# Kernel optimization log

Hardware: AMD Instinct MI355X
Metric: run time of the kernel (lower is better)

## Reference

```python
import jax, jax.numpy as jnp
import numpy as np

N = 100000        # vertices
E = 20000         # hyperedges
NNZ = 1000000     # incidence pairs
IN_CH = 128
HEADS = 8
OUT_CH = 16
D = HEADS * OUT_CH  # 128
NUM_TYPES = 16
K_CURV = 1.0      # Lorentz k = 1/c with c = 1


def lorentz_linear(x, W, b, scale_log):
    # HyboNet LorentzLinear: linear map, then project onto hyperboloid.
    y = x @ W.T + b                                   # [N, D]
    time = jax.nn.sigmoid(y[..., :1]) * jnp.exp(scale_log) + 1.1  # [N, 1]
    x_narrow = y[..., 1:]                             # [N, D-1]
    sq = jnp.sum(x_narrow * x_narrow, axis=-1, keepdims=True)
    scale = (time * time - K_CURV) / (sq + 1e-8)
    return jnp.concatenate([time, x_narrow * jnp.sqrt(scale)], axis=-1)


def setup_inputs() -> dict:
    key = jax.random.key(0)
    ks = jax.random.split(key, 8)
    X = jax.random.normal(ks[0], (N, IN_CH), dtype=jnp.float32)
    emb_ty = jax.random.normal(ks[1], (NUM_TYPES, D), dtype=jnp.float32)
    vertex = jax.random.randint(ks[2], (NNZ,), 0, N, dtype=jnp.int32)
    edges = jax.random.randint(ks[3], (NNZ,), 0, E, dtype=jnp.int32)
    type_ids = jax.random.randint(ks[4], (NNZ,), 0, NUM_TYPES, dtype=jnp.int32)
    # LorentzLinear params (nn.Linear with bias, scale init log(10))
    W = jax.random.normal(ks[5], (D, IN_CH), dtype=jnp.float32) / np.sqrt(IN_CH)
    b = jnp.zeros((D,), dtype=jnp.float32)
    scale_log = jnp.asarray(np.log(10.0), dtype=jnp.float32)
    eps = jnp.asarray([0.5], dtype=jnp.float32)
    return {"X": X, "emb_ty": emb_ty, "W": W, "b": b, "scale_log": scale_log,
            "eps": eps, "vertex": vertex, "edges": edges, "type_ids": type_ids,
            "num_edges": E}


def reference(X, emb_ty, W, b, scale_log, eps, vertex, edges, type_ids, num_edges):
    n = X.shape[0]
    Xh = lorentz_linear(X, W, b, scale_log)           # [N, D]
    Xve = Xh[vertex] - emb_ty[type_ids]               # [NNZ, D] gather + subtract
    Xe = jax.ops.segment_sum(Xve, edges, num_segments=num_edges)  # [E, D]
    Xev = Xe[edges]                                   # [NNZ, D]
    Xv = jax.ops.segment_sum(Xev, vertex, num_segments=n)         # [N, D]
    return eps * Xv + Xh
```

## Files before the change

kernel.cpp:

```cpp
#include <hip/hip_runtime.h>
#include <hip/hip_bf16.h>


#define E_SEGS 20000

__global__ __launch_bounds__(256) void lorentz_gemm_kernel(
    const float* __restrict__ X, const float* __restrict__ W,
    const float* __restrict__ bias, const float* __restrict__ scale_log,
    float* __restrict__ Xh, int N)
{
    __shared__ float4 Ws[128 * 32];
    __shared__ float4 Xs[64 * 33];
    const int t = threadIdx.x;

    #pragma unroll
    for (int i = 0; i < 16; ++i) {
        int f4 = t + i * 256;
        int d  = f4 >> 5;
        int c  = f4 & 31;
        Ws[d * 32 + (c ^ ((d >> 3) & 7))] = ((const float4*)W)[f4];
    }
    const int row0 = blockIdx.x * 64;
    #pragma unroll
    for (int i = 0; i < 8; ++i) {
        int f4 = t + i * 256;
        int r  = f4 >> 5;
        int c  = f4 & 31;
        int gr = row0 + r;
        float4 x = make_float4(0.f, 0.f, 0.f, 0.f);
        if (gr < N) x = ((const float4*)X)[(size_t)gr * 32 + c];
        Xs[r * 33 + c] = x;
    }
    __syncthreads();

    const int rg  = t >> 4;
    const int cg  = t & 15;
    const int r0  = rg << 2;
    const int swz = cg & 7;

    float acc[4][8];
    #pragma unroll
    for (int r = 0; r < 4; ++r)
        #pragma unroll
        for (int j = 0; j < 8; ++j) acc[r][j] = 0.f;

    #pragma unroll 2
    for (int k4 = 0; k4 < 32; ++k4) {
        float4 xq[4];
        #pragma unroll
        for (int rr = 0; rr < 4; ++rr) xq[rr] = Xs[(r0 + rr) * 33 + k4];
        float4 wq[8];
        const int kk = k4 ^ swz;
        #pragma unroll
        for (int j = 0; j < 8; ++j) wq[j] = Ws[(cg * 8 + j) * 32 + kk];
        #pragma unroll
        for (int rr = 0; rr < 4; ++rr)
            #pragma unroll
            for (int j = 0; j < 8; ++j)
                acc[rr][j] += xq[rr].x * wq[j].x + xq[rr].y * wq[j].y
                            + xq[rr].z * wq[j].z + xq[rr].w * wq[j].w;
    }

    const int cb = cg << 3;
    float4 b0 = ((const float4*)bias)[cg * 2];
    float4 b1 = ((const float4*)bias)[cg * 2 + 1];
    #pragma unroll
    for (int r = 0; r < 4; ++r) {
        acc[r][0] += b0.x; acc[r][1] += b0.y; acc[r][2] += b0.z; acc[r][3] += b0.w;
        acc[r][4] += b1.x; acc[r][5] += b1.y; acc[r][6] += b1.z; acc[r][7] += b1.w;
    }

    const float es = expf(scale_log[0]);

    #pragma unroll
    for (int r = 0; r < 4; ++r) {
        float sq = 0.f;
        #pragma unroll
        for (int j = 0; j < 8; ++j) sq += acc[r][j] * acc[r][j];
        if (cg == 0) sq -= acc[r][0] * acc[r][0];
        #pragma unroll
        for (int m = 1; m < 16; m <<= 1) sq += __shfl_xor(sq, m, 16);
        float y0   = __shfl(acc[r][0], 0, 16);
        float time = es / (1.f + expf(-y0)) + 1.1f;
        float ss   = sqrtf((time * time - 1.f) / (sq + 1e-8f));
        float4 o0, o1;
        o0.x = (cg == 0) ? time : acc[r][0] * ss;
        o0.y = acc[r][1] * ss; o0.z = acc[r][2] * ss; o0.w = acc[r][3] * ss;
        o1.x = acc[r][4] * ss; o1.y = acc[r][5] * ss;
        o1.z = acc[r][6] * ss; o1.w = acc[r][7] * ss;
        int grow = row0 + r0 + r;
        if (grow < N) {
            float4* ph = (float4*)(Xh + (size_t)grow * 128 + cb);
            ph[0] = o0; ph[1] = o1;
        }
    }
}

__global__ __launch_bounds__(256) void count_both_kernel(
    const int* __restrict__ edges, const int* __restrict__ vertex,
    int* __restrict__ hist_e, int* __restrict__ hist_v, int n)
{
    int i = blockIdx.x * 256 + threadIdx.x;
    if (i < n) {
        atomicAdd(&hist_e[edges[i]], 1);
        atomicAdd(&hist_v[vertex[i]], 1);
    }
}

__global__ __launch_bounds__(256) void scan_partial_kernel(
    const int* __restrict__ counts, int* __restrict__ offs,
    int* __restrict__ bsums, int n)
{
    __shared__ int buf[256];
    const int b = blockIdx.x, tid = threadIdx.x;
    const int i0 = b * 1024 + tid * 4;
    int c0 = (i0 + 0 < n) ? counts[i0 + 0] : 0;
    int c1 = (i0 + 1 < n) ? counts[i0 + 1] : 0;
    int c2 = (i0 + 2 < n) ? counts[i0 + 2] : 0;
    int c3 = (i0 + 3 < n) ? counts[i0 + 3] : 0;
    int s = c0 + c1 + c2 + c3;
    buf[tid] = s;
    __syncthreads();
    #pragma unroll
    for (int off = 1; off < 256; off <<= 1) {
        int v = (tid >= off) ? buf[tid - off] : 0;
        __syncthreads();
        buf[tid] += v;
        __syncthreads();
    }
    int ex = buf[tid] - s;
    if (i0 + 0 < n) offs[i0 + 0] = ex;
    if (i0 + 1 < n) offs[i0 + 1] = ex + c0;
    if (i0 + 2 < n) offs[i0 + 2] = ex + c0 + c1;
    if (i0 + 3 < n) offs[i0 + 3] = ex + c0 + c1 + c2;
    if (tid == 255) bsums[b] = buf[255];
}

__global__ __launch_bounds__(256) void scan_bsums_kernel(
    int* __restrict__ bsums, int nb)
{
    __shared__ int buf[256];
    const int tid = threadIdx.x;
    int v = (tid < nb) ? bsums[tid] : 0;
    buf[tid] = v;
    __syncthreads();
    #pragma unroll
    for (int off = 1; off < 256; off <<= 1) {
        int u = (tid >= off) ? buf[tid - off] : 0;
        __syncthreads();
        buf[tid] += u;
        __syncthreads();
    }
    if (tid < nb) bsums[tid] = buf[tid] - v;
}

__global__ __launch_bounds__(256) void scan_add_kernel(
    int* __restrict__ offs, const int* __restrict__ bsums, int n, int total)
{
    const int b = blockIdx.x, tid = threadIdx.x;
    const int add = bsums[b];
    const int i0 = b * 1024 + tid * 4;
    if (add != 0) {
        if (i0 + 0 < n) offs[i0 + 0] += add;
        if (i0 + 1 < n) offs[i0 + 1] += add;
        if (i0 + 2 < n) offs[i0 + 2] += add;
        if (i0 + 3 < n) offs[i0 + 3] += add;
    }
    if (b == 0 && tid == 0) offs[n] = total;
}

__global__ __launch_bounds__(256) void fill_both_kernel(
    const int* __restrict__ edges, const int* __restrict__ vertex,
    const int* __restrict__ types,
    const int* __restrict__ offs_e, int* __restrict__ cur_e,
    int* __restrict__ vals_e,
    const int* __restrict__ offs_v, int* __restrict__ cur_v,
    int* __restrict__ segs_v, int n)
{
    int i = blockIdx.x * 256 + threadIdx.x;
    if (i < n) {
        int s = edges[i];
        int v = vertex[i];
        int pe = atomicAdd(&cur_e[s], 1);
        vals_e[offs_e[s] + pe] = v | (types[i] << 17);
        int pv = atomicAdd(&cur_v[v], 1);
        segs_v[offs_v[v] + pv] = s;
    }
}

__global__ __launch_bounds__(256) void edge_gather_kernel(
    const float* __restrict__ Xh, const float* __restrict__ emb,
    const int* __restrict__ offs, const int* __restrict__ vals,
    float* __restrict__ Xe, int nsegs)
{
    int seg = blockIdx.x * 4 + (threadIdx.x >> 6);
    if (seg >= nsegs) return;
    const int lane = threadIdx.x & 63;
    const int h = lane >> 5, l5 = lane & 31;
    const int beg = offs[seg], end = offs[seg + 1];
    float4 acc = make_float4(0.f, 0.f, 0.f, 0.f);
    for (int e = beg + h; e < end; e += 2) {
        int p  = vals[e];
        int v  = p & 0x1FFFF, ty = p >> 17;
        float4 a = ((const float4*)Xh)[(size_t)v * 32 + l5];
        float4 m = ((const float4*)emb)[ty * 32 + l5];
        acc.x += a.x - m.x; acc.y += a.y - m.y;
        acc.z += a.z - m.z; acc.w += a.w - m.w;
    }
    acc.x += __shfl_xor(acc.x, 32);
    acc.y += __shfl_xor(acc.y, 32);
    acc.z += __shfl_xor(acc.z, 32);
    acc.w += __shfl_xor(acc.w, 32);
    if (h == 0) ((float4*)Xe)[(size_t)seg * 32 + l5] = acc;
}

__global__ __launch_bounds__(256) void vertex_gather_kernel(
    const float* __restrict__ Xh, const float* __restrict__ Xe,
    const int* __restrict__ offs, const int* __restrict__ segs,
    const float* __restrict__ eps, float* __restrict__ out, int N)
{
    int v = blockIdx.x * 4 + (threadIdx.x >> 6);
    if (v >= N) return;
    const int lane = threadIdx.x & 63;
    const int h = lane >> 5, l5 = lane & 31;
    const int beg = offs[v], end = offs[v + 1];
    float4 acc = make_float4(0.f, 0.f, 0.f, 0.f);
    for (int e = beg + h; e < end; e += 2) {
        int s = segs[e];
        float4 a = ((const float4*)Xe)[(size_t)s * 32 + l5];
        acc.x += a.x; acc.y += a.y; acc.z += a.z; acc.w += a.w;
    }
    acc.x += __shfl_xor(acc.x, 32);
    acc.y += __shfl_xor(acc.y, 32);
    acc.z += __shfl_xor(acc.z, 32);
    acc.w += __shfl_xor(acc.w, 32);
    if (h == 0) {
        float ep = eps[0];
        float4 xh = ((const float4*)Xh)[(size_t)v * 32 + l5];
        float4 o;
        o.x = xh.x + ep * acc.x; o.y = xh.y + ep * acc.y;
        o.z = xh.z + ep * acc.z; o.w = xh.w + ep * acc.w;
        ((float4*)out)[(size_t)v * 32 + l5] = o;
    }
}

extern "C" void kernel_launch(void* const* d_in, const int* in_sizes, int n_in,
                              void* d_out, int out_size, void* d_ws, size_t ws_size,
                              hipStream_t stream) {
    const float* X         = (const float*)d_in[0];
    const float* emb_ty    = (const float*)d_in[1];
    const float* W         = (const float*)d_in[2];
    const float* bias      = (const float*)d_in[3];
    const float* scale_log = (const float*)d_in[4];
    const float* eps       = (const float*)d_in[5];
    const int*   vertex    = (const int*)d_in[6];
    const int*   edges     = (const int*)d_in[7];
    const int*   type_ids  = (const int*)d_in[8];

    const int N   = in_sizes[0] / 128;
    const int nnz = in_sizes[6];
    const int E   = E_SEGS;

    float* Xh = (float*)d_ws;
    float* Xe = Xh + (size_t)N * 128;
    int* ip      = (int*)(Xe + (size_t)E * 128);
    int* offs_e  = ip;              ip += E + 1;
    int* offs_v  = ip;              ip += N + 1;
    int* hist_e  = ip;              ip += E;
    int* hist_v  = ip;              ip += N;
    int* cur_e   = ip;              ip += E;
    int* cur_v   = ip;              ip += N;
    int* bsum_e  = ip;              ip += 256;
    int* bsum_v  = ip;              ip += 256;
    int* vals_e  = ip;              ip += nnz;
    int* segs_v  = ip;              ip += nnz;

    hipMemsetAsync(hist_e, 0, (size_t)(2 * E + 2 * N) * sizeof(int), stream);

    float* out = (float*)d_out;
    const int blocks_nnz = (nnz + 255) / 256;
    const int nb_e = (E + 1023) / 1024;
    const int nb_v = (N + 1023) / 1024;

    count_both_kernel<<<blocks_nnz, 256, 0, stream>>>(
        edges, vertex, hist_e, hist_v, nnz);

    scan_partial_kernel<<<nb_e, 256, 0, stream>>>(hist_e, offs_e, bsum_e, E);
    scan_partial_kernel<<<nb_v, 256, 0, stream>>>(hist_v, offs_v, bsum_v, N);
    scan_bsums_kernel<<<1, 256, 0, stream>>>(bsum_e, nb_e);
    scan_bsums_kernel<<<1, 256, 0, stream>>>(bsum_v, nb_v);
    scan_add_kernel<<<nb_e, 256, 0, stream>>>(offs_e, bsum_e, E, nnz);
    scan_add_kernel<<<nb_v, 256, 0, stream>>>(offs_v, bsum_v, N, nnz);

    fill_both_kernel<<<blocks_nnz, 256, 0, stream>>>(
        edges, vertex, type_ids, offs_e, cur_e, vals_e, offs_v, cur_v,
        segs_v, nnz);

    lorentz_gemm_kernel<<<(N + 63) / 64, 256, 0, stream>>>(
        X, W, bias, scale_log, Xh, N);

    edge_gather_kernel<<<(E + 3) / 4, 256, 0, stream>>>(
        Xh, emb_ty, offs_e, vals_e, Xe, E);

    vertex_gather_kernel<<<(N + 3) / 4, 256, 0, stream>>>(
        Xh, Xe, offs_v, segs_v, eps, out, N);
}
```

Measured before the change: 574.6 us.

## Retile Lorentz GEMM to 128-row blocks with K-chunked smem; seed fill cursors from offsets

```diff
diff --git a/kernel.cpp b/kernel.cpp
--- a/kernel.cpp
+++ b/kernel.cpp
@@ -9,63 +9,64 @@
     const float* __restrict__ bias, const float* __restrict__ scale_log,
     float* __restrict__ Xh, int N)
 {
-    __shared__ float4 Ws[128 * 32];
-    __shared__ float4 Xs[64 * 33];
+    __shared__ float4 Ws[128 * 9];
+    __shared__ float4 Xs[128 * 9];
     const int t = threadIdx.x;
-
-    #pragma unroll
-    for (int i = 0; i < 16; ++i) {
-        int f4 = t + i * 256;
-        int d  = f4 >> 5;
-        int c  = f4 & 31;
-        Ws[d * 32 + (c ^ ((d >> 3) & 7))] = ((const float4*)W)[f4];
-    }
-    const int row0 = blockIdx.x * 64;
-    #pragma unroll
-    for (int i = 0; i < 8; ++i) {
-        int f4 = t + i * 256;
-        int r  = f4 >> 5;
-        int c  = f4 & 31;
-        int gr = row0 + r;
-        float4 x = make_float4(0.f, 0.f, 0.f, 0.f);
-        if (gr < N) x = ((const float4*)X)[(size_t)gr * 32 + c];
-        Xs[r * 33 + c] = x;
-    }
-    __syncthreads();
-
-    const int rg  = t >> 4;
-    const int cg  = t & 15;
-    const int r0  = rg << 2;
-    const int swz = cg & 7;
-
-    float acc[4][8];
-    #pragma unroll
-    for (int r = 0; r < 4; ++r)
+    const int row0 = blockIdx.x * 128;
+
+    const int rg = t >> 4;
+    const int cg = t & 15;
+    const int sr = t >> 3;
+    const int sc = t & 7;
+
+    float acc[8][8];
+    #pragma unroll
+    for (int r = 0; r < 8; ++r)
         #pragma unroll
         for (int j = 0; j < 8; ++j) acc[r][j] = 0.f;
 
-    #pragma unroll 2
-    for (int k4 = 0; k4 < 32; ++k4) {
-        float4 xq[4];
-        #pragma unroll
-        for (int rr = 0; rr < 4; ++rr) xq[rr] = Xs[(r0 + rr) * 33 + k4];
-        float4 wq[8];
-        const int kk = k4 ^ swz;
-        #pragma unroll
-        for (int j = 0; j < 8; ++j) wq[j] = Ws[(cg * 8 + j) * 32 + kk];
-        #pragma unroll
-        for (int rr = 0; rr < 4; ++rr)
+    for (int ch = 0; ch < 4; ++ch) {
+        if (ch) __syncthreads();
+        const int kb = ch * 8;
+        #pragma unroll
+        for (int i = 0; i < 4; ++i) {
+            int d = sr + i * 32;
+            Ws[d * 9 + (sc ^ ((d >> 3) & 7))] =
+                ((const float4*)W)[(size_t)d * 32 + kb + sc];
+        }
+        #pragma unroll
+        for (int i = 0; i < 4; ++i) {
+            int r = sr + i * 32;
+            int gr = row0 + r;
+            float4 x = make_float4(0.f, 0.f, 0.f, 0.f);
+            if (gr < N) x = ((const float4*)X)[(size_t)gr * 32 + kb + sc];
+            Xs[r * 9 + (sc ^ ((r >> 3) & 7))] = x;
+        }
+        __syncthreads();
+
+        #pragma unroll
+        for (int k4 = 0; k4 < 8; ++k4) {
+            float4 xq[8], wq[8];
+            const int xc = k4 ^ (rg & 7);
             #pragma unroll
-            for (int j = 0; j < 8; ++j)
-                acc[rr][j] += xq[rr].x * wq[j].x + xq[rr].y * wq[j].y
-                            + xq[rr].z * wq[j].z + xq[rr].w * wq[j].w;
+            for (int rr = 0; rr < 8; ++rr) xq[rr] = Xs[(rg * 8 + rr) * 9 + xc];
+            const int wc = k4 ^ (cg & 7);
+            #pragma unroll
+            for (int j = 0; j < 8; ++j) wq[j] = Ws[(cg * 8 + j) * 9 + wc];
+            #pragma unroll
+            for (int rr = 0; rr < 8; ++rr)
+                #pragma unroll
+                for (int j = 0; j < 8; ++j)
+                    acc[rr][j] += xq[rr].x * wq[j].x + xq[rr].y * wq[j].y
+                                + xq[rr].z * wq[j].z + xq[rr].w * wq[j].w;
+        }
     }
 
     const int cb = cg << 3;
     float4 b0 = ((const float4*)bias)[cg * 2];
     float4 b1 = ((const float4*)bias)[cg * 2 + 1];
     #pragma unroll
-    for (int r = 0; r < 4; ++r) {
+    for (int r = 0; r < 8; ++r) {
         acc[r][0] += b0.x; acc[r][1] += b0.y; acc[r][2] += b0.z; acc[r][3] += b0.w;
         acc[r][4] += b1.x; acc[r][5] += b1.y; acc[r][6] += b1.z; acc[r][7] += b1.w;
     }
@@ -73,7 +74,7 @@
     const float es = expf(scale_log[0]);
 
     #pragma unroll
-    for (int r = 0; r < 4; ++r) {
+    for (int r = 0; r < 8; ++r) {
         float sq = 0.f;
         #pragma unroll
         for (int j = 0; j < 8; ++j) sq += acc[r][j] * acc[r][j];
@@ -88,7 +89,7 @@
         o0.y = acc[r][1] * ss; o0.z = acc[r][2] * ss; o0.w = acc[r][3] * ss;
         o1.x = acc[r][4] * ss; o1.y = acc[r][5] * ss;
         o1.z = acc[r][6] * ss; o1.w = acc[r][7] * ss;
-        int grow = row0 + r0 + r;
+        int grow = row0 + (rg << 3) + r;
         if (grow < N) {
             float4* ph = (float4*)(Xh + (size_t)grow * 128 + cb);
             ph[0] = o0; ph[1] = o1;
@@ -172,19 +173,17 @@
 __global__ __launch_bounds__(256) void fill_both_kernel(
     const int* __restrict__ edges, const int* __restrict__ vertex,
     const int* __restrict__ types,
-    const int* __restrict__ offs_e, int* __restrict__ cur_e,
-    int* __restrict__ vals_e,
-    const int* __restrict__ offs_v, int* __restrict__ cur_v,
-    int* __restrict__ segs_v, int n)
+    int* __restrict__ cur_e, int* __restrict__ vals_e,
+    int* __restrict__ cur_v, int* __restrict__ segs_v, int n)
 {
     int i = blockIdx.x * 256 + threadIdx.x;
     if (i < n) {
         int s = edges[i];
         int v = vertex[i];
         int pe = atomicAdd(&cur_e[s], 1);
-        vals_e[offs_e[s] + pe] = v | (types[i] << 17);
+        vals_e[pe] = v | (types[i] << 17);
         int pv = atomicAdd(&cur_v[v], 1);
-        segs_v[offs_v[v] + pv] = s;
+        segs_v[pv] = s;
     }
 }
 
@@ -275,7 +274,7 @@
     int* vals_e  = ip;              ip += nnz;
     int* segs_v  = ip;              ip += nnz;
 
-    hipMemsetAsync(hist_e, 0, (size_t)(2 * E + 2 * N) * sizeof(int), stream);
+    hipMemsetAsync(hist_e, 0, (size_t)(E + N) * sizeof(int), stream);
 
     float* out = (float*)d_out;
     const int blocks_nnz = (nnz + 255) / 256;
@@ -292,11 +291,14 @@
     scan_add_kernel<<<nb_e, 256, 0, stream>>>(offs_e, bsum_e, E, nnz);
     scan_add_kernel<<<nb_v, 256, 0, stream>>>(offs_v, bsum_v, N, nnz);
 
+    hipMemcpyAsync(cur_e, offs_e, (size_t)E * sizeof(int),
+                   hipMemcpyDeviceToDevice, stream);
+    hipMemcpyAsync(cur_v, offs_v, (size_t)N * sizeof(int),
+                   hipMemcpyDeviceToDevice, stream);
     fill_both_kernel<<<blocks_nnz, 256, 0, stream>>>(
-        edges, vertex, type_ids, offs_e, cur_e, vals_e, offs_v, cur_v,
-        segs_v, nnz);
-
-    lorentz_gemm_kernel<<<(N + 63) / 64, 256, 0, stream>>>(
+        edges, vertex, type_ids, cur_e, vals_e, cur_v, segs_v, nnz);
+
+    lorentz_gemm_kernel<<<(N + 127) / 128, 256, 0, stream>>>(
         X, W, bias, scale_log, Xh, N);
 
     edge_gather_kernel<<<(E + 3) / 4, 256, 0, stream>>>(
```

Result: slower. 1.010 ms (+75.8%).
